# Kernel tuning notes

Hardware: AMD Instinct MI355X
Metric: run time of the kernel (lower is better)

The kernel has to match this reference:

```python
import jax, jax.numpy as jnp
import numpy as np

N_NODES = 50000
N_EDGES = 800000


def _inv_sqrt_deg(idx, n):
    deg = jax.ops.segment_sum(jnp.ones(idx.shape, jnp.float32), idx, num_segments=n)
    return jnp.where(deg > 0, deg ** -0.5, 0.0)


def graph_conv(x, W, b, src, dst, norm_src, norm_dst):
    # DGL GraphConv, norm='both': D_dst^{-1/2} A D_src^{-1/2} X W + b
    # Apply weight before aggregation (out_feats < in_feats in both layers).
    h = (x * norm_src[:, None]) @ W            # [N, out]
    m = h[src]                                  # gather per-edge messages [E, out]
    agg = jax.ops.segment_sum(m, dst, num_segments=x.shape[0])
    return agg * norm_dst[:, None] + b


def setup_inputs() -> dict:
    key = jax.random.key(0)
    ks = jax.random.split(key, 6)
    x = jax.random.normal(ks[0], (N_NODES, 512), jnp.float32)
    W1 = jax.random.normal(ks[1], (512, 128), jnp.float32) * (512 ** -0.5)
    b1 = jnp.zeros((128,), jnp.float32)
    W2 = jax.random.normal(ks[2], (128, 40), jnp.float32) * (128 ** -0.5)
    b2 = jnp.zeros((40,), jnp.float32)
    src = jax.random.randint(ks[3], (N_EDGES,), 0, N_NODES, jnp.int32)
    dst = jax.random.randint(ks[4], (N_EDGES,), 0, N_NODES, jnp.int32)
    return {"x": x, "W1": W1, "b1": b1, "W2": W2, "b2": b2, "src": src, "dst": dst}


def reference(x, W1, b1, W2, b2, src, dst):
    n = x.shape[0]
    norm_src = _inv_sqrt_deg(src, n)  # out-degree based src norm
    norm_dst = _inv_sqrt_deg(dst, n)  # in-degree based dst norm
    h = graph_conv(x, W1, b1, src, dst, norm_src, norm_dst)
    h = jax.nn.relu(h)
    h = graph_conv(h, W2, b2, src, dst, norm_src, norm_dst)
    return h
```

## Files before the change

### kernel.cpp

```cpp
#include <hip/hip_runtime.h>
#include <hip/hip_bf16.h>

#define F0 512
#define F1 128
#define F2 40

#define NRP 12800
#define G_SL 64

typedef __attribute__((ext_vector_type(8))) short bf16x8;
typedef __attribute__((ext_vector_type(4))) float f32x4;

__device__ inline ushort f2bf(float f) {
    union { float f; uint u; } v; v.f = f;
    uint u = v.u;
    uint r = u + 0x7fffu + ((u >> 16) & 1u);
    return (ushort)(r >> 16);
}

#define CVT2(dst, a, b) { __hip_bfloat162 _t2 = __float22bfloat162_rn(make_float2(a, b)); __builtin_memcpy(&dst, &_t2, 4); }

__global__ __launch_bounds__(1024)
void hist_kernel(const int* __restrict__ src, const int* __restrict__ dst,
                 ushort* __restrict__ Gsrc, ushort* __restrict__ Gdst,
                 const float* __restrict__ W1, ushort* __restrict__ Wt, int n, int E) {
    if (blockIdx.x < (F0 * F1) / 1024) {
        int idx = blockIdx.x * 1024 + threadIdx.x;
        int k = idx >> 7, nn = idx & 127;
        Wt[nn * F0 + k] = f2bf(W1[idx]);
    }
    __shared__ uint cs[NRP / 2];
    __shared__ uint cd[NRP / 2];
    const int p = blockIdx.x / G_SL;
    const int g = blockIdx.x % G_SL;
    const int base = p * NRP;
    for (int i = threadIdx.x; i < NRP / 2; i += 1024) { cs[i] = 0; cd[i] = 0; }
    __syncthreads();
    const int Epg = (E + G_SL - 1) / G_SL;
    const int e0 = g * Epg;
    const int e1 = min(E, e0 + Epg);
    for (int i = e0 + (int)threadIdx.x; i < e1; i += 1024) {
        int s = src[i], d = dst[i];
        unsigned so = (unsigned)(s - base);
        unsigned dd = (unsigned)(d - base);
        if (so < (unsigned)NRP) atomicAdd(&cs[so >> 1], 1u << ((so & 1) * 16));
        if (dd < (unsigned)NRP) atomicAdd(&cd[dd >> 1], 1u << ((dd & 1) * 16));
    }
    __syncthreads();
    const int lim = min(NRP, n - base);
    for (int i = threadIdx.x; i < lim; i += 1024) {
        uint pcs = cs[i >> 1], pcd = cd[i >> 1];
        int sh = (i & 1) * 16;
        Gsrc[(size_t)g * n + base + i] = (ushort)((pcs >> sh) & 0xffffu);
        Gdst[(size_t)g * n + base + i] = (ushort)((pcd >> sh) & 0xffffu);
    }
}

__global__ __launch_bounds__(256)
void scanA_kernel(const ushort* __restrict__ Gsrc, const ushort* __restrict__ Gdst,
                  float* __restrict__ norm_src, float* __restrict__ norm_dst,
                  int* __restrict__ row_off, int* __restrict__ bsum, int n) {
    __shared__ int sm[256];
    int i = blockIdx.x * 256 + threadIdx.x;
    int s = 0, d = 0;
    if (i < n) {
#pragma unroll
        for (int g = 0; g < G_SL; g++) {
            s += Gsrc[(size_t)g * n + i];
            d += Gdst[(size_t)g * n + i];
        }
        norm_src[i] = s > 0 ? rsqrtf((float)s) : 0.f;
        norm_dst[i] = d > 0 ? rsqrtf((float)d) : 0.f;
    }
    sm[threadIdx.x] = (i < n) ? d : 0;
    __syncthreads();
    for (int off = 1; off < 256; off <<= 1) {
        int t = (threadIdx.x >= (unsigned)off) ? sm[threadIdx.x - off] : 0;
        __syncthreads();
        sm[threadIdx.x] += t;
        __syncthreads();
    }
    if (i < n) row_off[i + 1] = sm[threadIdx.x];
    if (threadIdx.x == 255) bsum[blockIdx.x] = sm[255];
}

__global__ __launch_bounds__(256)
void finalize_kernel(int* __restrict__ row_off, const int* __restrict__ bsum,
                     const ushort* __restrict__ Gdst, int* __restrict__ Goff, int n) {
    __shared__ int sm[256];
    const int b = blockIdx.x;
    const int t = threadIdx.x;
    sm[t] = (t < b) ? bsum[t] : 0;
    __syncthreads();
#pragma unroll
    for (int off = 128; off > 0; off >>= 1) {
        if (t < off) sm[t] += sm[t + off];
        __syncthreads();
    }
    const int excl = sm[0];
    const int v = b * 256 + t;
    if (v >= n) return;
    int raw = row_off[v];
    int start = excl + ((t == 0) ? 0 : raw);
    if (v == n - 1) {
        int rawn = row_off[n];
        row_off[n] = excl + rawn;
    }
    row_off[v] = start;
    int run = start;
#pragma unroll
    for (int g = 0; g < G_SL; g++) {
        size_t idx = (size_t)g * n + v;
        Goff[idx] = run;
        run += Gdst[idx];
    }
}

__global__ __launch_bounds__(1024)
void place_kernel(const int* __restrict__ src, const int* __restrict__ dst,
                  const int* __restrict__ Goff, int* __restrict__ edge_src, int n, int E) {
    __shared__ int cur[NRP];
    const int p = blockIdx.x / G_SL;
    const int g = blockIdx.x % G_SL;
    const int base = p * NRP;
    const int lim = min(NRP, n - base);
    for (int i = threadIdx.x; i < lim; i += 1024)
        cur[i] = Goff[(size_t)g * n + base + i];
    __syncthreads();
    const int Epg = (E + G_SL - 1) / G_SL;
    const int e0 = g * Epg;
    const int e1 = min(E, e0 + Epg);
    for (int i = e0 + (int)threadIdx.x; i < e1; i += 1024) {
        int d = dst[i];
        unsigned dd = (unsigned)(d - base);
        if (dd < (unsigned)lim) {
            int pos = atomicAdd(&cur[dd], 1);
            edge_src[pos] = src[i];
        }
    }
}

#define BM 64

#define LOADT(f, i, kto) {                                                             \
    int _r = (i) * 16 + (tid >> 5);                                                    \
    f = (bm + _r < n) ? *reinterpret_cast<const float4*>(                              \
            x + (size_t)(bm + _r) * F0 + (kto) * 128 + (tid & 31) * 4)                 \
                      : make_float4(0.f, 0.f, 0.f, 0.f); }

#define STAGEW(bufp, i, f) {                                                           \
    int _r = (i) * 16 + (tid >> 5);                                                    \
    int _c4 = tid & 31;                                                                \
    uint _h0, _h1;                                                                     \
    CVT2(_h0, f.x, f.y); CVT2(_h1, f.z, f.w);                                          \
    int _byte = _r * 256 + ((((_c4) >> 1) ^ (_r & 7)) << 4) + ((_c4 & 1) << 3);        \
    *reinterpret_cast<uint2*>((bufp) + _byte) = make_uint2(_h0, _h1); }

#define LOADB(k0, b) { b = *reinterpret_cast<const bf16x8*>(bp + (k0)); }

#define COMPUTE(bufp, kt2, b) {                                                        \
    const int _cx = ((((kt2) * 4) + lq) ^ (l15 & 7)) << 4;                             \
    const char* _pb = (bufp) + l15 * 256 + _cx;                                        \
    bf16x8 _a0 = *reinterpret_cast<const bf16x8*>(_pb + 0 * 4096);                     \
    bf16x8 _a1 = *reinterpret_cast<const bf16x8*>(_pb + 1 * 4096);                     \
    bf16x8 _a2 = *reinterpret_cast<const bf16x8*>(_pb + 2 * 4096);                     \
    bf16x8 _a3 = *reinterpret_cast<const bf16x8*>(_pb + 3 * 4096);                     \
    acc[0] = __builtin_amdgcn_mfma_f32_16x16x32_bf16(_a0, b, acc[0], 0, 0, 0);         \
    acc[1] = __builtin_amdgcn_mfma_f32_16x16x32_bf16(_a1, b, acc[1], 0, 0, 0);         \
    acc[2] = __builtin_amdgcn_mfma_f32_16x16x32_bf16(_a2, b, acc[2], 0, 0, 0);         \
    acc[3] = __builtin_amdgcn_mfma_f32_16x16x32_bf16(_a3, b, acc[3], 0, 0, 0); }

__global__ __launch_bounds__(512)
void gemm1_mfma(const float* __restrict__ x, const ushort* __restrict__ Wt,
                const float* __restrict__ norm_src, ushort* __restrict__ h1g, int n) {
    __shared__ __align__(16) char Al[2][16384];

    const int tid = threadIdx.x;
    const int lane = tid & 63;
    const int w = tid >> 6;
    const int l15 = lane & 15;
    const int lq = lane >> 4;
    const int bm = blockIdx.x * BM;
    (void)lane;

    const ushort* bp = Wt + (size_t)(w * 16 + l15) * F0 + lq * 8;

    f32x4 acc[4] = {};
    float4 f0, f1, f2, f3;
    bf16x8 bcur, bnxt;

    LOADB(0, bcur);
    LOADT(f0, 0, 0); LOADT(f1, 1, 0); LOADT(f2, 2, 0); LOADT(f3, 3, 0);
    STAGEW(&Al[0][0], 0, f0); STAGEW(&Al[0][0], 1, f1);
    STAGEW(&Al[0][0], 2, f2); STAGEW(&Al[0][0], 3, f3);
    __syncthreads();

    for (int kto = 0; kto < 4; ++kto) {
        const int cb = kto & 1;
        char* bufp = &Al[cb][0];
        if (kto < 3) {
            LOADT(f0, 0, kto + 1); LOADT(f1, 1, kto + 1);
            LOADT(f2, 2, kto + 1); LOADT(f3, 3, kto + 1);
        }
#pragma unroll
        for (int kt2 = 0; kt2 < 4; ++kt2) {
            const int kg = kto * 4 + kt2;
            const int knxt = (kg + 1 < 16) ? (kg + 1) : 15;
            LOADB(knxt * 32, bnxt);
            COMPUTE(bufp, kt2, bcur);
            bcur = bnxt;
        }
        if (kto < 3) {
            char* nbufp = &Al[cb ^ 1][0];
            STAGEW(nbufp, 0, f0); STAGEW(nbufp, 1, f1);
            STAGEW(nbufp, 2, f2); STAGEW(nbufp, 3, f3);
            __syncthreads();
        }
    }

#pragma unroll
    for (int mi = 0; mi < 4; mi++) {
        int rbase = bm + mi * 16 + lq * 4;
#pragma unroll
        for (int r = 0; r < 4; r++) {
            int row = rbase + r;
            if (row < n) {
                float ns = norm_src[row];
                h1g[(size_t)row * F1 + w * 16 + l15] = f2bf(acc[mi][r] * ns);
            }
        }
    }
}

__global__ __launch_bounds__(256)
void agg1_kernel(const ushort* __restrict__ h1g, const int* __restrict__ row_off,
                 const int* __restrict__ edge_src, const float* __restrict__ norm_dst,
                 const float* __restrict__ b1, ushort* __restrict__ h1, int n) {
    int wid = (blockIdx.x * blockDim.x + threadIdx.x) >> 6;
    int lane = threadIdx.x & 63;
    if (wid >= n) return;
    int beg = row_off[wid], end = row_off[wid + 1];
    float a0 = 0.f, a1 = 0.f;
    int e = beg;
    for (; e + 7 < end; e += 8) {
        int s[8];
#pragma unroll
        for (int j = 0; j < 8; j++) s[j] = edge_src[e + j];
        uint v[8];
#pragma unroll
        for (int j = 0; j < 8; j++)
            v[j] = *reinterpret_cast<const uint*>(&h1g[(size_t)s[j] * F1 + lane * 2]);
#pragma unroll
        for (int j = 0; j < 8; j++) {
            a0 += __uint_as_float(v[j] << 16);
            a1 += __uint_as_float(v[j] & 0xffff0000u);
        }
    }
    for (; e < end; ++e) {
        int s = edge_src[e];
        uint v = *reinterpret_cast<const uint*>(&h1g[(size_t)s * F1 + lane * 2]);
        a0 += __uint_as_float(v << 16);
        a1 += __uint_as_float(v & 0xffff0000u);
    }
    float nd = norm_dst[wid];
    float o0 = fmaxf(a0 * nd + b1[lane * 2 + 0], 0.f);
    float o1 = fmaxf(a1 * nd + b1[lane * 2 + 1], 0.f);
    __hip_bfloat162 p2 = __float22bfloat162_rn(make_float2(o0, o1));
    uint pu; __builtin_memcpy(&pu, &p2, 4);
    *reinterpret_cast<uint*>(&h1[(size_t)wid * F1 + lane * 2]) = pu;
}

__global__ __launch_bounds__(256)
void gemm2_kernel(const ushort* __restrict__ h1, const float* __restrict__ W2,
                  const float* __restrict__ norm_src, ushort* __restrict__ h2g, int n) {
    __shared__ __align__(16) float W2s[F1][F2];
    for (int i = threadIdx.x; i < F1 * F2; i += 256)
        W2s[i / F2][i % F2] = W2[i];
    __syncthreads();
    int node = blockIdx.x * 256 + threadIdx.x;
    if (node >= n) return;
    float nrm = norm_src[node];
    f32x4 acc4[10] = {};
    const ushort* row = &h1[(size_t)node * F1];
    for (int kc = 0; kc < 16; kc++) {
        uint4 u = *reinterpret_cast<const uint4*>(&row[kc * 8]);
        uint uu[4] = {u.x, u.y, u.z, u.w};
        float f[8];
#pragma unroll
        for (int i = 0; i < 4; i++) {
            f[2 * i + 0] = __uint_as_float(uu[i] << 16);
            f[2 * i + 1] = __uint_as_float(uu[i] & 0xffff0000u);
        }
#pragma unroll
        for (int j = 0; j < 8; j++) {
#pragma unroll
            for (int c4 = 0; c4 < 10; c4++) {
                f32x4 wv = *reinterpret_cast<const f32x4*>(&W2s[kc * 8 + j][c4 * 4]);
                acc4[c4] += f[j] * wv;
            }
        }
    }
    ushort* orow = &h2g[(size_t)node * F2];
#pragma unroll
    for (int c4 = 0; c4 < 10; c4++) {
        f32x4 o = acc4[c4] * nrm;
        __hip_bfloat162 pa = __float22bfloat162_rn(make_float2(o[0], o[1]));
        __hip_bfloat162 pb = __float22bfloat162_rn(make_float2(o[2], o[3]));
        uint2 pk;
        __builtin_memcpy(&pk.x, &pa, 4);
        __builtin_memcpy(&pk.y, &pb, 4);
        *reinterpret_cast<uint2*>(&orow[c4 * 4]) = pk;
    }
}

__global__ __launch_bounds__(256)
void agg2_kernel(const ushort* __restrict__ h2g, const int* __restrict__ row_off,
                 const int* __restrict__ edge_src, const float* __restrict__ norm_dst,
                 const float* __restrict__ b2, float* __restrict__ out, int n) {
    int wid = (blockIdx.x * blockDim.x + threadIdx.x) >> 6;
    int lane = threadIdx.x & 63;
    if (wid >= n) return;
    int beg = row_off[wid], end = row_off[wid + 1];
    float a0 = 0.f, a1 = 0.f;
    int e = beg;
    const bool act = lane < 20;
    for (; e + 7 < end; e += 8) {
        int s[8];
#pragma unroll
        for (int j = 0; j < 8; j++) s[j] = edge_src[e + j];
        if (act) {
            uint v[8];
#pragma unroll
            for (int j = 0; j < 8; j++)
                v[j] = *reinterpret_cast<const uint*>(&h2g[(size_t)s[j] * F2 + lane * 2]);
#pragma unroll
            for (int j = 0; j < 8; j++) {
                a0 += __uint_as_float(v[j] << 16);
                a1 += __uint_as_float(v[j] & 0xffff0000u);
            }
        }
    }
    for (; e < end; ++e) {
        int s = edge_src[e];
        if (act) {
            uint v = *reinterpret_cast<const uint*>(&h2g[(size_t)s * F2 + lane * 2]);
            a0 += __uint_as_float(v << 16);
            a1 += __uint_as_float(v & 0xffff0000u);
        }
    }
    if (act) {
        float nd = norm_dst[wid];
        float o0 = a0 * nd + b2[lane * 2 + 0];
        float o1 = a1 * nd + b2[lane * 2 + 1];
        *reinterpret_cast<float2*>(&out[(size_t)wid * F2 + lane * 2]) = make_float2(o0, o1);
    }
}

extern "C" void kernel_launch(void* const* d_in, const int* in_sizes, int n_in,
                              void* d_out, int out_size, void* d_ws, size_t ws_size,
                              hipStream_t stream) {
    const float* x  = (const float*)d_in[0];
    const float* W1 = (const float*)d_in[1];
    const float* b1 = (const float*)d_in[2];
    const float* W2 = (const float*)d_in[3];
    const float* b2 = (const float*)d_in[4];
    const int* src  = (const int*)d_in[5];
    const int* dst  = (const int*)d_in[6];
    float* out = (float*)d_out;

    const int n = in_sizes[0] / F0;
    const int E = in_sizes[5];
    const int nb = (n + 255) / 256;
    const int P = (n + NRP - 1) / NRP;

    char* ws = (char*)d_ws;
    auto alloc = [&](size_t bytes) -> char* {
        char* p = ws;
        ws += (bytes + 255) & ~(size_t)255;
        return p;
    };
    int* row_off   = (int*)alloc((size_t)(n + 1) * 4);
    int* bsum      = (int*)alloc(256 * 4);
    int* edge_srcs = (int*)alloc((size_t)E * 4);
    float* norm_src_d = (float*)alloc((size_t)n * 4);
    float* norm_dst_d = (float*)alloc((size_t)n * 4);
    ushort* W1t = (ushort*)alloc((size_t)F1 * F0 * 2);
    ushort* h1g = (ushort*)alloc((size_t)n * F1 * 2);
    ushort* h1  = (ushort*)alloc((size_t)n * F1 * 2);
    ushort* h2g = h1g;

    ushort* Gsrc = (ushort*)h1g;
    ushort* Gdst = Gsrc + (size_t)G_SL * n;
    int* Goff = (int*)h1;

    hist_kernel<<<P * G_SL, 1024, 0, stream>>>(src, dst, Gsrc, Gdst, W1, W1t, n, E);
    scanA_kernel<<<nb, 256, 0, stream>>>(Gsrc, Gdst, norm_src_d, norm_dst_d, row_off, bsum, n);
    finalize_kernel<<<nb, 256, 0, stream>>>(row_off, bsum, Gdst, Goff, n);
    place_kernel<<<P * G_SL, 1024, 0, stream>>>(src, dst, Goff, edge_srcs, n, E);
    gemm1_mfma<<<(n + BM - 1) / BM, 512, 0, stream>>>(x, W1t, norm_src_d, h1g, n);
    agg1_kernel<<<(n + 3) / 4, 256, 0, stream>>>(h1g, row_off, edge_srcs, norm_dst_d, b1, h1, n);
    gemm2_kernel<<<(n + 255) / 256, 256, 0, stream>>>(h1, W2, norm_src_d, h2g, n);
    agg2_kernel<<<(n + 3) / 4, 256, 0, stream>>>(h2g, row_off, edge_srcs, norm_dst_d, b2, out, n);
}
```

Measured before the change: 187.3 us.

## Stage gemm1 A tiles via direct global-to-LDS loads with fp32 in LDS

Replaces the register-staged load, bf16 convert and swizzled LDS store of x tiles with global_load_lds DMA of raw fp32 into a double-buffered 32-column LDS tile. The bf16 conversion moves to fragment construction right before the MFMA. The intent is to cut VGPR pressure and staging instructions and to overlap global loads with compute. In exchange there are 16 barriers per block instead of 4, the conversion work is duplicated across the waves that read each fragment, and there may be a wait-count issue because nothing explicitly waits on vmcnt for the async LDS writes before the barrier.

```diff
diff --git a/kernel.cpp b/kernel.cpp
--- a/kernel.cpp
+++ b/kernel.cpp
@@ -142,29 +142,28 @@
 
 #define BM 64
 
-#define LOADT(f, i, kto) {                                                             \
-    int _r = (i) * 16 + (tid >> 5);                                                    \
-    f = (bm + _r < n) ? *reinterpret_cast<const float4*>(                              \
-            x + (size_t)(bm + _r) * F0 + (kto) * 128 + (tid & 31) * 4)                 \
-                      : make_float4(0.f, 0.f, 0.f, 0.f); }
-
-#define STAGEW(bufp, i, f) {                                                           \
-    int _r = (i) * 16 + (tid >> 5);                                                    \
-    int _c4 = tid & 31;                                                                \
-    uint _h0, _h1;                                                                     \
-    CVT2(_h0, f.x, f.y); CVT2(_h1, f.z, f.w);                                          \
-    int _byte = _r * 256 + ((((_c4) >> 1) ^ (_r & 7)) << 4) + ((_c4 & 1) << 3);        \
-    *reinterpret_cast<uint2*>((bufp) + _byte) = make_uint2(_h0, _h1); }
+#define ISSUE(kt, buf) {                                                               \
+    __builtin_amdgcn_global_load_lds(                                                  \
+        (const __attribute__((address_space(1))) void*)(gsrc_base + (kt) * 32),        \
+        (__attribute__((address_space(3))) void*)(&Al[buf][tid * 16]),                 \
+        16, 0, 0); }
 
 #define LOADB(k0, b) { b = *reinterpret_cast<const bf16x8*>(bp + (k0)); }
 
-#define COMPUTE(bufp, kt2, b) {                                                        \
-    const int _cx = ((((kt2) * 4) + lq) ^ (l15 & 7)) << 4;                             \
-    const char* _pb = (bufp) + l15 * 256 + _cx;                                        \
-    bf16x8 _a0 = *reinterpret_cast<const bf16x8*>(_pb + 0 * 4096);                     \
-    bf16x8 _a1 = *reinterpret_cast<const bf16x8*>(_pb + 1 * 4096);                     \
-    bf16x8 _a2 = *reinterpret_cast<const bf16x8*>(_pb + 2 * 4096);                     \
-    bf16x8 _a3 = *reinterpret_cast<const bf16x8*>(_pb + 3 * 4096);                     \
+#define MKFRAG(dst, mi, bufp) {                                                        \
+    const int _row = (mi) * 16 + l15;                                                  \
+    const char* _pr = (bufp) + _row * 128;                                             \
+    float4 _pa = *reinterpret_cast<const float4*>(_pr + (((2 * lq + 0) ^ (_row & 7)) << 4)); \
+    float4 _pb = *reinterpret_cast<const float4*>(_pr + (((2 * lq + 1) ^ (_row & 7)) << 4)); \
+    union { uint u[4]; bf16x8 v; } _pk;                                                \
+    CVT2(_pk.u[0], _pa.x, _pa.y); CVT2(_pk.u[1], _pa.z, _pa.w);                        \
+    CVT2(_pk.u[2], _pb.x, _pb.y); CVT2(_pk.u[3], _pb.z, _pb.w);                        \
+    dst = _pk.v; }
+
+#define COMPUTE(buf, b) {                                                              \
+    const char* _bp = &Al[buf][0];                                                     \
+    bf16x8 _a0, _a1, _a2, _a3;                                                         \
+    MKFRAG(_a0, 0, _bp); MKFRAG(_a1, 1, _bp); MKFRAG(_a2, 2, _bp); MKFRAG(_a3, 3, _bp);\
     acc[0] = __builtin_amdgcn_mfma_f32_16x16x32_bf16(_a0, b, acc[0], 0, 0, 0);         \
     acc[1] = __builtin_amdgcn_mfma_f32_16x16x32_bf16(_a1, b, acc[1], 0, 0, 0);         \
     acc[2] = __builtin_amdgcn_mfma_f32_16x16x32_bf16(_a2, b, acc[2], 0, 0, 0);         \
@@ -173,7 +172,7 @@
 __global__ __launch_bounds__(512)
 void gemm1_mfma(const float* __restrict__ x, const ushort* __restrict__ Wt,
                 const float* __restrict__ norm_src, ushort* __restrict__ h1g, int n) {
-    __shared__ __align__(16) char Al[2][16384];
+    __shared__ __align__(16) char Al[2][8192];
 
     const int tid = threadIdx.x;
     const int lane = tid & 63;
@@ -181,41 +180,31 @@
     const int l15 = lane & 15;
     const int lq = lane >> 4;
     const int bm = blockIdx.x * BM;
-    (void)lane;
+
+    const int st_r = tid >> 3;
+    const int st_c = (tid & 7) ^ (st_r & 7);
+    int grow = bm + st_r;
+    if (grow >= n) grow = n - 1;
+    const float* gsrc_base = x + (size_t)grow * F0 + st_c * 4;
 
     const ushort* bp = Wt + (size_t)(w * 16 + l15) * F0 + lq * 8;
 
     f32x4 acc[4] = {};
-    float4 f0, f1, f2, f3;
     bf16x8 bcur, bnxt;
 
+    ISSUE(0, 0);
     LOADB(0, bcur);
-    LOADT(f0, 0, 0); LOADT(f1, 1, 0); LOADT(f2, 2, 0); LOADT(f3, 3, 0);
-    STAGEW(&Al[0][0], 0, f0); STAGEW(&Al[0][0], 1, f1);
-    STAGEW(&Al[0][0], 2, f2); STAGEW(&Al[0][0], 3, f3);
-    __syncthreads();
-
-    for (int kto = 0; kto < 4; ++kto) {
-        const int cb = kto & 1;
-        char* bufp = &Al[cb][0];
-        if (kto < 3) {
-            LOADT(f0, 0, kto + 1); LOADT(f1, 1, kto + 1);
-            LOADT(f2, 2, kto + 1); LOADT(f3, 3, kto + 1);
-        }
-#pragma unroll
-        for (int kt2 = 0; kt2 < 4; ++kt2) {
-            const int kg = kto * 4 + kt2;
-            const int knxt = (kg + 1 < 16) ? (kg + 1) : 15;
-            LOADB(knxt * 32, bnxt);
-            COMPUTE(bufp, kt2, bcur);
-            bcur = bnxt;
-        }
-        if (kto < 3) {
-            char* nbufp = &Al[cb ^ 1][0];
-            STAGEW(nbufp, 0, f0); STAGEW(nbufp, 1, f1);
-            STAGEW(nbufp, 2, f2); STAGEW(nbufp, 3, f3);
-            __syncthreads();
-        }
+    __syncthreads();
+
+    for (int kg = 0; kg < 16; ++kg) {
+        const int cb = kg & 1;
+        if (kg < 15) {
+            ISSUE(kg + 1, cb ^ 1);
+            LOADB((kg + 1) * 32, bnxt);
+        }
+        COMPUTE(cb, bcur);
+        bcur = bnxt;
+        if (kg < 15) __syncthreads();
     }
 
 #pragma unroll
```

Result: faster. 179.0 us (-4.4%).
